# Kernel optimization log

Hardware: AMD Instinct MI355X
Metric: run time of the kernel (lower is better)

The kernel has to match this reference:

```python
import jax, jax.numpy as jnp
import numpy as np
from jax import lax

L, E, H, V, B, S = 25, 64, 8, 30000, 1000, 512


def setup_inputs() -> dict:
    key = jax.random.key(0)
    ks = jax.random.split(key, 24)
    p = lambda k, shape: (jax.random.normal(k, shape) * 0.1).astype(jnp.float32)
    inp = {
        "x": jax.random.randint(ks[0], (B, S), 0, V),
        "embedding": p(ks[1], (V, E)),
        # layer 0 (input dim = E)
        "W_xz0": p(ks[2], (E, H)), "W_hz0": p(ks[3], (H, H)), "b_z0": p(ks[4], (H,)),
        "W_xr0": p(ks[5], (E, H)), "W_hr0": p(ks[6], (H, H)), "b_r0": p(ks[7], (H,)),
        "W_xH0": p(ks[8], (E, H)), "W_rH0": p(ks[9], (H, H)), "b_H0": p(ks[10], (H,)),
        # layers 1..L-1 stacked (input dim = H)
        "W_xz": p(ks[11], (L - 1, H, H)), "W_hz": p(ks[12], (L - 1, H, H)), "b_z": p(ks[13], (L - 1, H)),
        "W_xr": p(ks[14], (L - 1, H, H)), "W_hr": p(ks[15], (L - 1, H, H)), "b_r": p(ks[16], (L - 1, H)),
        "W_xH": p(ks[17], (L - 1, H, H)), "W_rH": p(ks[18], (L - 1, H, H)), "b_H": p(ks[19], (L - 1, H)),
        "W_hy": p(ks[20], (H, 1)), "b_y": p(ks[21], (1,)),
    }
    return inp


def _cell(x_t, h, Wxz, Whz, bz, Wxr, Whr, br, WxH, WrH, bH):
    z = jax.nn.sigmoid(x_t @ Wxz + h @ Whz + bz)
    r = jax.nn.sigmoid(x_t @ Wxr + h @ Whr + br)
    Hc = jnp.tanh(x_t @ WxH + (h * r) @ WrH + bH)
    return h * (1.0 - z) + z * Hc


def reference(x, embedding, W_xz0, W_hz0, b_z0, W_xr0, W_hr0, b_r0, W_xH0, W_rH0, b_H0,
              W_xz, W_hz, b_z, W_xr, W_hr, b_r, W_xH, W_rH, b_H, W_hy, b_y):
    emb = embedding[x]                     # [B, S, E]
    bsz = x.shape[0]
    h0 = jnp.zeros((L, bsz, H), dtype=embedding.dtype)

    def time_step(h_all, x_t):            # h_all: [L, B, H]; x_t: [B, E]
        h_new0 = _cell(x_t, h_all[0], W_xz0, W_hz0, b_z0, W_xr0, W_hr0, b_r0, W_xH0, W_rH0, b_H0)

        def layer_step(inp_t, ws):
            Wxz, Whz, bz, Wxr, Whr, br, WxH, WrH, bH, h_prev = ws
            h_new = _cell(inp_t, h_prev, Wxz, Whz, bz, Wxr, Whr, br, WxH, WrH, bH)
            return h_new, h_new

        _, h_rest = lax.scan(layer_step, h_new0,
                             (W_xz, W_hz, b_z, W_xr, W_hr, b_r, W_xH, W_rH, b_H, h_all[1:]))
        return jnp.concatenate([h_new0[None], h_rest], axis=0), None

    h_last, _ = lax.scan(time_step, h0, jnp.swapaxes(emb, 0, 1))  # scan over S
    logits = h_last[-1] @ W_hy + b_y       # [B, 1]
    return logits.squeeze(-1), h_last
```

## Files before the change

kernel.cpp:

```cpp
#include <hip/hip_runtime.h>
#include <hip/hip_bf16.h>
#include <stdint.h>

#define L_ 25
#define E_ 64
#define H_ 8
#define B_ 1000
#define S_ 512
#define GQ 4
#define NCELL (L_ * GQ)
#define TPBR (NCELL * 8)
#define NSUPER (S_ / 2 + L_ - 1)
#define HS 12
#define XG 20

typedef float v2f __attribute__((ext_vector_type(2)));
typedef float v4f __attribute__((ext_vector_type(4)));

#define PIN(x) asm volatile("" : "+v"(x))

__device__ __forceinline__ v2f pkfma(v2f a, v2f b, v2f c) {
  v2f d;
  asm("v_pk_fma_f32 %0, %1, %2, %3" : "=v"(d) : "v"(a), "v"(b), "v"(c));
  return d;
}
__device__ __forceinline__ v2f vlo(v4f v) { return __builtin_shufflevector(v, v, 0, 1); }
__device__ __forceinline__ v2f vhi(v4f v) { return __builtin_shufflevector(v, v, 2, 3); }
__device__ __forceinline__ v2f mk2(float a, float b) { v2f r; r.x = a; r.y = b; return r; }

__device__ __forceinline__ float ulo(uint32_t u) { return __uint_as_float(u << 16); }
__device__ __forceinline__ float uhi(uint32_t u) { return __uint_as_float(u & 0xffff0000u); }

__device__ __forceinline__ float toF(float v) { return v; }
__device__ __forceinline__ float toF(__hip_bfloat16 v) { return __bfloat162float(v); }
__device__ __forceinline__ void stP(float* p, float v) { *p = v; }
__device__ __forceinline__ void stP(__hip_bfloat16* p, float v) { *p = __float2bfloat16(v); }

__device__ __forceinline__ void load8f(const __hip_bfloat16* p, float* o) {
  const uint4 v = *(const uint4*)p;
  o[0] = ulo(v.x); o[1] = uhi(v.x); o[2] = ulo(v.y); o[3] = uhi(v.y);
  o[4] = ulo(v.z); o[5] = uhi(v.z); o[6] = ulo(v.w); o[7] = uhi(v.w);
}
__device__ __forceinline__ void load8f(const float* p, float* o) {
  const float4 a = ((const float4*)p)[0];
  const float4 b = ((const float4*)p)[1];
  o[0] = a.x; o[1] = a.y; o[2] = a.z; o[3] = a.w;
  o[4] = b.x; o[5] = b.y; o[6] = b.z; o[7] = b.w;
}

__device__ __forceinline__ void st4(float* p, float a, float b, float c, float d) {
  float4 v; v.x = a; v.y = b; v.z = c; v.w = d;
  *(float4*)p = v;
}
__device__ __forceinline__ void st4(__hip_bfloat16* p, float a, float b, float c, float d) {
  __hip_bfloat16 t[4] = {__float2bfloat16(a), __float2bfloat16(b),
                         __float2bfloat16(c), __float2bfloat16(d)};
  *(ushort4*)p = *(ushort4*)t;
}

__device__ __forceinline__ float sigmo(float x) {
  return __builtin_amdgcn_rcpf(1.f + __expf(-x));
}
__device__ __forceinline__ float tanh_(float x) {
  x = fminf(fmaxf(x, -15.f), 15.f);
  const float e = __expf(-2.f * x);
  return (1.f - e) * __builtin_amdgcn_rcpf(1.f + e);
}

__global__ void gru_detect(const unsigned short* __restrict__ u16, int* __restrict__ flag) {
  const int i = threadIdx.x;
  float m = 0.f;
#pragma unroll
  for (int k = 0; k < 4; ++k) {
    const uint32_t u = u16[i * 4 + k];
    float v = fabsf(__uint_as_float(u << 16));
    if (!(v < 1e30f)) v = 1e30f;
    m = fmaxf(m, v);
  }
#pragma unroll
  for (int off = 32; off; off >>= 1) m = fmaxf(m, __shfl_down(m, off, 64));
  if (i == 0) *flag = (m > 2.0f) ? 0 : 1;
}

template <typename T, typename PT>
__global__ __launch_bounds__(256, 4) void gru_pre(
    const int* __restrict__ flag, int want,
    const int* __restrict__ x, const T* __restrict__ emb,
    const T* __restrict__ Wz, const T* __restrict__ Wr,
    const T* __restrict__ Wh, PT* __restrict__ pre) {
  if (*flag != want) return;
  __shared__ __align__(16) float WL[64 * 24];
  __shared__ __align__(16) float TB[4][24 * 65];
  for (int idx = threadIdx.x; idx < 64 * 24; idx += 256) {
    const int k = idx / 24, c = idx - k * 24;
    const T* src = (c < 8) ? Wz : ((c < 16) ? Wr : Wh);
    WL[idx] = toF(src[k * 8 + (c & 7)]);
  }
  __syncthreads();

  const int tok = blockIdx.x * 256 + threadIdx.x;
  const int t = x[tok];

  v2f acc[12];
#pragma unroll
  for (int q = 0; q < 12; ++q) acc[q] = mk2(0.f, 0.f);

  for (int kb = 0; kb < 8; ++kb) {
    float e[8];
    load8f(emb + (size_t)t * E_ + kb * 8, e);
#pragma unroll
    for (int k8 = 0; k8 < 8; ++k8) {
      const v4f* wr = (const v4f*)(WL + (kb * 8 + k8) * 24);
      const v2f ee = mk2(e[k8], e[k8]);
#pragma unroll
      for (int q = 0; q < 6; ++q) {
        const v4f w4 = wr[q];
        acc[2 * q]     = pkfma(ee, vlo(w4), acc[2 * q]);
        acc[2 * q + 1] = pkfma(ee, vhi(w4), acc[2 * q + 1]);
      }
    }
  }

  const int wid = threadIdx.x >> 6, lane = threadIdx.x & 63;
  float* tb = &TB[wid][0];
#pragma unroll
  for (int q = 0; q < 12; ++q) {
    tb[(2 * q) * 65 + lane] = acc[q].x;
    tb[(2 * q + 1) * 65 + lane] = acc[q].y;
  }
  asm volatile("s_waitcnt lgkmcnt(0)" ::: "memory");
  __builtin_amdgcn_wave_barrier();

  PT* ob = pre + (size_t)(blockIdx.x * 256 + wid * 64) * 24;
#pragma unroll
  for (int it = 0; it < 6; ++it) {
    const int F0 = it * 256 + lane * 4;
    float o[4];
#pragma unroll
    for (int e2 = 0; e2 < 4; ++e2) {
      const int F = F0 + e2;
      const int tk = F / 24;
      const int c = F - tk * 24;
      o[e2] = tb[c * 65 + tk];
    }
    st4(ob + F0, o[0], o[1], o[2], o[3]);
  }
}

template <typename T, typename PT>
__global__ __launch_bounds__(TPBR, 4) void gru_rec(
    const int* __restrict__ flag, int want,
    const PT* __restrict__ pre,
    const T* __restrict__ Whz0, const T* __restrict__ bz0,
    const T* __restrict__ Whr0, const T* __restrict__ br0,
    const T* __restrict__ WrH0, const T* __restrict__ bH0,
    const T* __restrict__ Wxz, const T* __restrict__ Whz,
    const T* __restrict__ bz, const T* __restrict__ Wxr,
    const T* __restrict__ Whr, const T* __restrict__ br,
    const T* __restrict__ WxH, const T* __restrict__ WrH,
    const T* __restrict__ bH, const T* __restrict__ Why,
    const T* __restrict__ by, T* __restrict__ out) {
  if (*flag != want) return;
  __shared__ __align__(16) float hsh[NCELL * HS];
  __shared__ __align__(16) float hrsh[NCELL * HS];
  __shared__ __align__(16) float xbuf[2 * NCELL * XG];

  const int tid = threadIdx.x;
  const int gi = tid >> 3;
  const int j = tid & 7;
  const int l = gi >> 2;
  const int g = gi & 3;
  const int b = blockIdx.x * GQ + g;

  for (int i = tid; i < NCELL * HS; i += TPBR) { hsh[i] = 0.f; hrsh[i] = 0.f; }
  for (int i = tid; i < 2 * NCELL * XG; i += TPBR) xbuf[i] = 0.f;

  v2f wxz2[4], whz2[4], wxr2[4], whr2[4], wxh2[4], wrh2[4];
  v2f bz2, br2, bh2;
  if (l == 0) {
#pragma unroll
    for (int q = 0; q < 4; ++q) {
      whz2[q] = mk2(toF(Whz0[(2 * q) * 8 + j]), toF(Whz0[(2 * q + 1) * 8 + j]));
      whr2[q] = mk2(toF(Whr0[(2 * q) * 8 + j]), toF(Whr0[(2 * q + 1) * 8 + j]));
      wrh2[q] = mk2(toF(WrH0[(2 * q) * 8 + j]), toF(WrH0[(2 * q + 1) * 8 + j]));
      wxz2[q] = mk2(0.f, 0.f); wxr2[q] = mk2(0.f, 0.f); wxh2[q] = mk2(0.f, 0.f);
    }
    bz2 = mk2(toF(bz0[j]), 0.f);
    br2 = mk2(toF(br0[j]), 0.f);
    bh2 = mk2(toF(bH0[j]), 0.f);
  } else {
    const int base = (l - 1) * 64;
#pragma unroll
    for (int q = 0; q < 4; ++q) {
      wxz2[q] = mk2(toF(Wxz[base + (2 * q) * 8 + j]), toF(Wxz[base + (2 * q + 1) * 8 + j]));
      whz2[q] = mk2(toF(Whz[base + (2 * q) * 8 + j]), toF(Whz[base + (2 * q + 1) * 8 + j]));
      wxr2[q] = mk2(toF(Wxr[base + (2 * q) * 8 + j]), toF(Wxr[base + (2 * q + 1) * 8 + j]));
      whr2[q] = mk2(toF(Whr[base + (2 * q) * 8 + j]), toF(Whr[base + (2 * q + 1) * 8 + j]));
      wxh2[q] = mk2(toF(WxH[base + (2 * q) * 8 + j]), toF(WxH[base + (2 * q + 1) * 8 + j]));
      wrh2[q] = mk2(toF(WrH[base + (2 * q) * 8 + j]), toF(WrH[base + (2 * q + 1) * 8 + j]));
    }
    bz2 = mk2(toF(bz[(l - 1) * 8 + j]), 0.f);
    br2 = mk2(toF(br[(l - 1) * 8 + j]), 0.f);
    bh2 = mk2(toF(bH[(l - 1) * 8 + j]), 0.f);
  }
#pragma unroll
  for (int q = 0; q < 4; ++q) {
    PIN(wxz2[q]); PIN(whz2[q]); PIN(wxr2[q]); PIN(whr2[q]); PIN(wxh2[q]); PIN(wrh2[q]);
  }
  PIN(bz2); PIN(br2); PIN(bh2);

  const PT* ppr = pre + (size_t)b * (S_ * 24) + j;
  float cz0 = 0.f, cr0 = 0.f, ch0 = 0.f, cz1 = 0.f, cr1 = 0.f, ch1 = 0.f;
  if (l == 0) {
    cz0 = toF(ppr[0]);  cr0 = toF(ppr[8]);  ch0 = toF(ppr[16]);
    cz1 = toF(ppr[24]); cr1 = toF(ppr[32]); ch1 = toF(ppr[40]);
  }

  float* hgw = hsh + gi * HS;
  float* hrg = hrsh + gi * HS;
  float* hgwj = hgw + j;
  float* hrgj = hrg + j;
  const int gp = (gi >= GQ) ? (gi - GQ) * XG : 0;
  const float* xpe = xbuf + NCELL * XG + gp;
  const float* xpo = xbuf + gp;
  float* xce = xbuf + gi * XG;
  float* xco = xbuf + NCELL * XG + gi * XG;

  float hown = 0.f;

  __syncthreads();

  for (int s = 0; s < NSUPER; ++s) {
    const unsigned rel = (unsigned)(s - l);
    if (rel < (unsigned)(S_ / 2)) {
      const float* xp = (s & 1) ? xpo : xpe;
      float* xc = (s & 1) ? xco : xce;

      const v4f xa0 = ((const v4f*)xp)[0];
      const v4f xb0 = ((const v4f*)xp)[1];
      v2f azp = pkfma(vlo(xa0), wxz2[0], bz2);
      azp = pkfma(vhi(xa0), wxz2[1], azp);
      azp = pkfma(vlo(xb0), wxz2[2], azp);
      azp = pkfma(vhi(xb0), wxz2[3], azp);
      v2f arp = pkfma(vlo(xa0), wxr2[0], br2);
      arp = pkfma(vhi(xa0), wxr2[1], arp);
      arp = pkfma(vlo(xb0), wxr2[2], arp);
      arp = pkfma(vhi(xb0), wxr2[3], arp);
      v2f ahp = pkfma(vlo(xa0), wxh2[0], bh2);
      ahp = pkfma(vhi(xa0), wxh2[1], ahp);
      ahp = pkfma(vlo(xb0), wxh2[2], ahp);
      ahp = pkfma(vhi(xb0), wxh2[3], ahp);
      {
        const v4f h01 = ((const v4f*)hgw)[0];
        const v4f h23 = ((const v4f*)hgw)[1];
        azp = pkfma(vlo(h01), whz2[0], azp);
        azp = pkfma(vhi(h01), whz2[1], azp);
        azp = pkfma(vlo(h23), whz2[2], azp);
        azp = pkfma(vhi(h23), whz2[3], azp);
        arp = pkfma(vlo(h01), whr2[0], arp);
        arp = pkfma(vhi(h01), whr2[1], arp);
        arp = pkfma(vlo(h23), whr2[2], arp);
        arp = pkfma(vhi(h23), whr2[3], arp);
      }
      const float az0 = azp.x + azp.y + cz0;
      const float ar0 = arp.x + arp.y + cr0;
      const float zA = sigmo(az0);
      const float rA = sigmo(ar0);
      *hrgj = hown * rA;
      __builtin_amdgcn_wave_barrier();
      {
        const v4f r01 = ((const v4f*)hrg)[0];
        const v4f r23 = ((const v4f*)hrg)[1];
        ahp = pkfma(vlo(r01), wrh2[0], ahp);
        ahp = pkfma(vhi(r01), wrh2[1], ahp);
        ahp = pkfma(vlo(r23), wrh2[2], ahp);
        ahp = pkfma(vhi(r23), wrh2[3], ahp);
      }
      const float ah0 = ahp.x + ahp.y + ch0;
      const float hn0 = fmaf(zA, tanh_(ah0) - hown, hown);
      *hgwj = hn0;
      __builtin_amdgcn_wave_barrier();

      float pz0 = 0.f, pr0 = 0.f, ph0 = 0.f, pz1 = 0.f, pr1 = 0.f, ph1 = 0.f;
      const bool pf = (l == 0) && (rel + 1u < (unsigned)(S_ / 2));
      if (pf) {
        const PT* pn = ppr + (rel + 1) * 48;
        pz0 = toF(pn[0]);  pr0 = toF(pn[8]);  ph0 = toF(pn[16]);
        pz1 = toF(pn[24]); pr1 = toF(pn[32]); ph1 = toF(pn[40]);
      }
      const v4f xa1 = ((const v4f*)xp)[2];
      const v4f xb1 = ((const v4f*)xp)[3];
      v2f azp1 = pkfma(vlo(xa1), wxz2[0], bz2);
      azp1 = pkfma(vhi(xa1), wxz2[1], azp1);
      azp1 = pkfma(vlo(xb1), wxz2[2], azp1);
      azp1 = pkfma(vhi(xb1), wxz2[3], azp1);
      v2f arp1 = pkfma(vlo(xa1), wxr2[0], br2);
      arp1 = pkfma(vhi(xa1), wxr2[1], arp1);
      arp1 = pkfma(vlo(xb1), wxr2[2], arp1);
      arp1 = pkfma(vhi(xb1), wxr2[3], arp1);
      v2f ahp1 = pkfma(vlo(xa1), wxh2[0], bh2);
      ahp1 = pkfma(vhi(xa1), wxh2[1], ahp1);
      ahp1 = pkfma(vlo(xb1), wxh2[2], ahp1);
      ahp1 = pkfma(vhi(xb1), wxh2[3], ahp1);
      {
        const v4f h01 = ((const v4f*)hgw)[0];
        const v4f h23 = ((const v4f*)hgw)[1];
        azp1 = pkfma(vlo(h01), whz2[0], azp1);
        azp1 = pkfma(vhi(h01), whz2[1], azp1);
        azp1 = pkfma(vlo(h23), whz2[2], azp1);
        azp1 = pkfma(vhi(h23), whz2[3], azp1);
        arp1 = pkfma(vlo(h01), whr2[0], arp1);
        arp1 = pkfma(vhi(h01), whr2[1], arp1);
        arp1 = pkfma(vlo(h23), whr2[2], arp1);
        arp1 = pkfma(vhi(h23), whr2[3], arp1);
      }
      const float az1 = azp1.x + azp1.y + cz1;
      const float ar1 = arp1.x + arp1.y + cr1;
      const float zB = sigmo(az1);
      const float rB = sigmo(ar1);
      *hrgj = hn0 * rB;
      __builtin_amdgcn_wave_barrier();
      {
        const v4f r01 = ((const v4f*)hrg)[0];
        const v4f r23 = ((const v4f*)hrg)[1];
        ahp1 = pkfma(vlo(r01), wrh2[0], ahp1);
        ahp1 = pkfma(vhi(r01), wrh2[1], ahp1);
        ahp1 = pkfma(vlo(r23), wrh2[2], ahp1);
        ahp1 = pkfma(vhi(r23), wrh2[3], ahp1);
      }
      const float ah1 = ahp1.x + ahp1.y + ch1;
      const float hn1 = fmaf(zB, tanh_(ah1) - hn0, hn0);
      *hgwj = hn1;
      __builtin_amdgcn_wave_barrier();
      hown = hn1;

      xc[j] = hn0;
      xc[8 + j] = hn1;
      if (pf) { cz0 = pz0; cr0 = pr0; ch0 = ph0; cz1 = pz1; cr1 = pr1; ch1 = ph1; }
    }
    __syncthreads();
  }

  stP(out + B_ + (l * B_ + b) * H_ + j, hown);
  if (l == L_ - 1 && j == 0) {
    float ssum = toF(by[0]);
#pragma unroll
    for (int k = 0; k < 8; ++k) ssum = fmaf(hgw[k], toF(Why[k]), ssum);
    stP(out + b, ssum);
  }
}

template <typename T, typename PT>
static void launch_mode(const int* flag, int want, void* const* d_in, PT* pre,
                        T* out, hipStream_t stream) {
  const int* x = (const int*)d_in[0];
  const T* emb = (const T*)d_in[1];
  const T* Wxz0 = (const T*)d_in[2];
  const T* Whz0 = (const T*)d_in[3];
  const T* bz0 = (const T*)d_in[4];
  const T* Wxr0 = (const T*)d_in[5];
  const T* Whr0 = (const T*)d_in[6];
  const T* br0 = (const T*)d_in[7];
  const T* WxH0 = (const T*)d_in[8];
  const T* WrH0 = (const T*)d_in[9];
  const T* bH0 = (const T*)d_in[10];
  const T* Wxz = (const T*)d_in[11];
  const T* Whz = (const T*)d_in[12];
  const T* bz = (const T*)d_in[13];
  const T* Wxr = (const T*)d_in[14];
  const T* Whr = (const T*)d_in[15];
  const T* br = (const T*)d_in[16];
  const T* WxH = (const T*)d_in[17];
  const T* WrH = (const T*)d_in[18];
  const T* bH = (const T*)d_in[19];
  const T* Why = (const T*)d_in[20];
  const T* by = (const T*)d_in[21];

  gru_pre<T, PT><<<B_ * S_ / 256, 256, 0, stream>>>(flag, want, x, emb,
                                                    Wxz0, Wxr0, WxH0, pre);
  gru_rec<T, PT><<<B_ / GQ, TPBR, 0, stream>>>(
      flag, want, pre, Whz0, bz0, Whr0, br0, WrH0, bH0, Wxz, Whz, bz, Wxr, Whr,
      br, WxH, WrH, bH, Why, by, out);
}

extern "C" void kernel_launch(void* const* d_in, const int* in_sizes, int n_in,
                              void* d_out, int out_size, void* d_ws, size_t ws_size,
                              hipStream_t stream) {
  int* flag = (int*)d_ws;
  char* preMem = (char*)d_ws + 256;
  const size_t needF = (size_t)B_ * S_ * 24 * sizeof(float) + 256;

  gru_detect<<<1, 64, 0, stream>>>((const unsigned short*)d_in[1], flag);

  if (ws_size >= needF) {
    float* pre = (float*)preMem;
    launch_mode<float, float>(flag, 0, d_in, pre, (float*)d_out, stream);
    launch_mode<__hip_bfloat16, float>(flag, 1, d_in, pre, (__hip_bfloat16*)d_out, stream);
  } else {
    __hip_bfloat16* pre = (__hip_bfloat16*)preMem;
    launch_mode<float, __hip_bfloat16>(flag, 0, d_in, pre, (float*)d_out, stream);
    launch_mode<__hip_bfloat16, __hip_bfloat16>(flag, 1, d_in, pre, (__hip_bfloat16*)d_out, stream);
  }
}
```

Measured before the change: 415.6 us.

## Halve batch per block, restructure GRU step scheduling, simplify tanh

Cuts batch rows per block from 4 to 2, doubling the block count to 500 and halving per-block thread count. This spreads the serial wavefront over more CUs. The two-timestep inner body is reordered so all input projections for both steps are issued up front, and the r-gate path is computed before z to shorten the critical dependency chain. One wave barrier is dropped and tanh now uses 2*sigmoid(2x)-1 without clamping. Removing the clamp risks inf/NaN-free behaviour only through rcp saturation. The smaller blocks also change shared-memory layout size and how parallelism maps to waves.

```diff
diff --git a/kernel.cpp b/kernel.cpp
--- a/kernel.cpp
+++ b/kernel.cpp
@@ -7,7 +7,7 @@
 #define H_ 8
 #define B_ 1000
 #define S_ 512
-#define GQ 4
+#define GQ 2
 #define NCELL (L_ * GQ)
 #define TPBR (NCELL * 8)
 #define NSUPER (S_ / 2 + L_ - 1)
@@ -62,9 +62,8 @@
   return __builtin_amdgcn_rcpf(1.f + __expf(-x));
 }
 __device__ __forceinline__ float tanh_(float x) {
-  x = fminf(fmaxf(x, -15.f), 15.f);
   const float e = __expf(-2.f * x);
-  return (1.f - e) * __builtin_amdgcn_rcpf(1.f + e);
+  return fmaf(2.f, __builtin_amdgcn_rcpf(1.f + e), -1.f);
 }
 
 __global__ void gru_detect(const unsigned short* __restrict__ u16, int* __restrict__ flag) {
@@ -168,8 +167,8 @@
   const int tid = threadIdx.x;
   const int gi = tid >> 3;
   const int j = tid & 7;
-  const int l = gi >> 2;
-  const int g = gi & 3;
+  const int l = gi >> 1;
+  const int g = gi & 1;
   const int b = blockIdx.x * GQ + g;
 
   for (int i = tid; i < NCELL * HS; i += TPBR) { hsh[i] = 0.f; hrsh[i] = 0.f; }
@@ -236,50 +235,12 @@
       const float* xp = (s & 1) ? xpo : xpe;
       float* xc = (s & 1) ? xco : xce;
 
+      const v4f h01 = ((const v4f*)hgw)[0];
+      const v4f h23 = ((const v4f*)hgw)[1];
       const v4f xa0 = ((const v4f*)xp)[0];
       const v4f xb0 = ((const v4f*)xp)[1];
-      v2f azp = pkfma(vlo(xa0), wxz2[0], bz2);
-      azp = pkfma(vhi(xa0), wxz2[1], azp);
-      azp = pkfma(vlo(xb0), wxz2[2], azp);
-      azp = pkfma(vhi(xb0), wxz2[3], azp);
-      v2f arp = pkfma(vlo(xa0), wxr2[0], br2);
-      arp = pkfma(vhi(xa0), wxr2[1], arp);
-      arp = pkfma(vlo(xb0), wxr2[2], arp);
-      arp = pkfma(vhi(xb0), wxr2[3], arp);
-      v2f ahp = pkfma(vlo(xa0), wxh2[0], bh2);
-      ahp = pkfma(vhi(xa0), wxh2[1], ahp);
-      ahp = pkfma(vlo(xb0), wxh2[2], ahp);
-      ahp = pkfma(vhi(xb0), wxh2[3], ahp);
-      {
-        const v4f h01 = ((const v4f*)hgw)[0];
-        const v4f h23 = ((const v4f*)hgw)[1];
-        azp = pkfma(vlo(h01), whz2[0], azp);
-        azp = pkfma(vhi(h01), whz2[1], azp);
-        azp = pkfma(vlo(h23), whz2[2], azp);
-        azp = pkfma(vhi(h23), whz2[3], azp);
-        arp = pkfma(vlo(h01), whr2[0], arp);
-        arp = pkfma(vhi(h01), whr2[1], arp);
-        arp = pkfma(vlo(h23), whr2[2], arp);
-        arp = pkfma(vhi(h23), whr2[3], arp);
-      }
-      const float az0 = azp.x + azp.y + cz0;
-      const float ar0 = arp.x + arp.y + cr0;
-      const float zA = sigmo(az0);
-      const float rA = sigmo(ar0);
-      *hrgj = hown * rA;
-      __builtin_amdgcn_wave_barrier();
-      {
-        const v4f r01 = ((const v4f*)hrg)[0];
-        const v4f r23 = ((const v4f*)hrg)[1];
-        ahp = pkfma(vlo(r01), wrh2[0], ahp);
-        ahp = pkfma(vhi(r01), wrh2[1], ahp);
-        ahp = pkfma(vlo(r23), wrh2[2], ahp);
-        ahp = pkfma(vhi(r23), wrh2[3], ahp);
-      }
-      const float ah0 = ahp.x + ahp.y + ch0;
-      const float hn0 = fmaf(zA, tanh_(ah0) - hown, hown);
-      *hgwj = hn0;
-      __builtin_amdgcn_wave_barrier();
+      const v4f xa1 = ((const v4f*)xp)[2];
+      const v4f xb1 = ((const v4f*)xp)[3];
 
       float pz0 = 0.f, pr0 = 0.f, ph0 = 0.f, pz1 = 0.f, pr1 = 0.f, ph1 = 0.f;
       const bool pf = (l == 0) && (rel + 1u < (unsigned)(S_ / 2));
@@ -288,54 +249,89 @@
         pz0 = toF(pn[0]);  pr0 = toF(pn[8]);  ph0 = toF(pn[16]);
         pz1 = toF(pn[24]); pr1 = toF(pn[32]); ph1 = toF(pn[40]);
       }
-      const v4f xa1 = ((const v4f*)xp)[2];
-      const v4f xb1 = ((const v4f*)xp)[3];
+
+      v2f arh = pkfma(vlo(h01), whr2[0], mk2(0.f, 0.f));
+      arh = pkfma(vhi(h01), whr2[1], arh);
+      arh = pkfma(vlo(h23), whr2[2], arh);
+      arh = pkfma(vhi(h23), whr2[3], arh);
+      v2f azh = pkfma(vlo(h01), whz2[0], mk2(0.f, 0.f));
+      azh = pkfma(vhi(h01), whz2[1], azh);
+      azh = pkfma(vlo(h23), whz2[2], azh);
+      azh = pkfma(vhi(h23), whz2[3], azh);
+
+      v2f arp = pkfma(vlo(xa0), wxr2[0], br2);
+      arp = pkfma(vhi(xa0), wxr2[1], arp);
+      arp = pkfma(vlo(xb0), wxr2[2], arp);
+      arp = pkfma(vhi(xb0), wxr2[3], arp);
+      v2f azp = pkfma(vlo(xa0), wxz2[0], bz2);
+      azp = pkfma(vhi(xa0), wxz2[1], azp);
+      azp = pkfma(vlo(xb0), wxz2[2], azp);
+      azp = pkfma(vhi(xb0), wxz2[3], azp);
+      v2f ahp = pkfma(vlo(xa0), wxh2[0], bh2);
+      ahp = pkfma(vhi(xa0), wxh2[1], ahp);
+      ahp = pkfma(vlo(xb0), wxh2[2], ahp);
+      ahp = pkfma(vhi(xb0), wxh2[3], ahp);
+
+      v2f arp1 = pkfma(vlo(xa1), wxr2[0], br2);
+      arp1 = pkfma(vhi(xa1), wxr2[1], arp1);
+      arp1 = pkfma(vlo(xb1), wxr2[2], arp1);
+      arp1 = pkfma(vhi(xb1), wxr2[3], arp1);
       v2f azp1 = pkfma(vlo(xa1), wxz2[0], bz2);
       azp1 = pkfma(vhi(xa1), wxz2[1], azp1);
       azp1 = pkfma(vlo(xb1), wxz2[2], azp1);
       azp1 = pkfma(vhi(xb1), wxz2[3], azp1);
-      v2f arp1 = pkfma(vlo(xa1), wxr2[0], br2);
-      arp1 = pkfma(vhi(xa1), wxr2[1], arp1);
-      arp1 = pkfma(vlo(xb1), wxr2[2], arp1);
-      arp1 = pkfma(vhi(xb1), wxr2[3], arp1);
       v2f ahp1 = pkfma(vlo(xa1), wxh2[0], bh2);
       ahp1 = pkfma(vhi(xa1), wxh2[1], ahp1);
       ahp1 = pkfma(vlo(xb1), wxh2[2], ahp1);
       ahp1 = pkfma(vhi(xb1), wxh2[3], ahp1);
-      {
-        const v4f h01 = ((const v4f*)hgw)[0];
-        const v4f h23 = ((const v4f*)hgw)[1];
-        azp1 = pkfma(vlo(h01), whz2[0], azp1);
-        azp1 = pkfma(vhi(h01), whz2[1], azp1);
-        azp1 = pkfma(vlo(h23), whz2[2], azp1);
-        azp1 = pkfma(vhi(h23), whz2[3], azp1);
-        arp1 = pkfma(vlo(h01), whr2[0], arp1);
-        arp1 = pkfma(vhi(h01), whr2[1], arp1);
-        arp1 = pkfma(vlo(h23), whr2[2], arp1);
-        arp1 = pkfma(vhi(h23), whr2[3], arp1);
-      }
-      const float az1 = azp1.x + azp1.y + cz1;
+
+      const float ar0 = (arp.x + arp.y) + (arh.x + arh.y) + cr0;
+      const float rA = sigmo(ar0);
+      *hrgj = hown * rA;
+      __builtin_amdgcn_wave_barrier();
+
+      const v4f r01 = ((const v4f*)hrg)[0];
+      const v4f r23 = ((const v4f*)hrg)[1];
+      const float az0 = (azp.x + azp.y) + (azh.x + azh.y) + cz0;
+      const float zA = sigmo(az0);
+      ahp = pkfma(vlo(r01), wrh2[0], ahp);
+      ahp = pkfma(vhi(r01), wrh2[1], ahp);
+      ahp = pkfma(vlo(r23), wrh2[2], ahp);
+      ahp = pkfma(vhi(r23), wrh2[3], ahp);
+      const float ah0 = ahp.x + ahp.y + ch0;
+      const float hn0 = fmaf(zA, tanh_(ah0) - hown, hown);
+      *hgwj = hn0;
+      xc[j] = hn0;
+      __builtin_amdgcn_wave_barrier();
+
+      const v4f g01 = ((const v4f*)hgw)[0];
+      const v4f g23 = ((const v4f*)hgw)[1];
+      arp1 = pkfma(vlo(g01), whr2[0], arp1);
+      arp1 = pkfma(vhi(g01), whr2[1], arp1);
+      arp1 = pkfma(vlo(g23), whr2[2], arp1);
+      arp1 = pkfma(vhi(g23), whr2[3], arp1);
+      azp1 = pkfma(vlo(g01), whz2[0], azp1);
+      azp1 = pkfma(vhi(g01), whz2[1], azp1);
+      azp1 = pkfma(vlo(g23), whz2[2], azp1);
+      azp1 = pkfma(vhi(g23), whz2[3], azp1);
       const float ar1 = arp1.x + arp1.y + cr1;
-      const float zB = sigmo(az1);
       const float rB = sigmo(ar1);
       *hrgj = hn0 * rB;
       __builtin_amdgcn_wave_barrier();
-      {
-        const v4f r01 = ((const v4f*)hrg)[0];
-        const v4f r23 = ((const v4f*)hrg)[1];
-        ahp1 = pkfma(vlo(r01), wrh2[0], ahp1);
-        ahp1 = pkfma(vhi(r01), wrh2[1], ahp1);
-        ahp1 = pkfma(vlo(r23), wrh2[2], ahp1);
-        ahp1 = pkfma(vhi(r23), wrh2[3], ahp1);
-      }
+
+      const v4f q01 = ((const v4f*)hrg)[0];
+      const v4f q23 = ((const v4f*)hrg)[1];
+      const float az1 = azp1.x + azp1.y + cz1;
+      const float zB = sigmo(az1);
+      ahp1 = pkfma(vlo(q01), wrh2[0], ahp1);
+      ahp1 = pkfma(vhi(q01), wrh2[1], ahp1);
+      ahp1 = pkfma(vlo(q23), wrh2[2], ahp1);
+      ahp1 = pkfma(vhi(q23), wrh2[3], ahp1);
       const float ah1 = ahp1.x + ahp1.y + ch1;
       const float hn1 = fmaf(zB, tanh_(ah1) - hn0, hn0);
       *hgwj = hn1;
-      __builtin_amdgcn_wave_barrier();
+      xc[8 + j] = hn1;
       hown = hn1;
-
-      xc[j] = hn0;
-      xc[8 + j] = hn1;
       if (pf) { cz0 = pz0; cr0 = pr0; ch0 = ph0; cz1 = pz1; cr1 = pr1; ch1 = ph1; }
     }
     __syncthreads();
```

Measured after the change: 416.7 us. About the same (+0.3%).
